# Optimization experiments

Hardware: AMD Instinct MI355X
Metric: run time of the kernel (lower is better)

## Reference

```python
import jax, jax.numpy as jnp
import numpy as np

B, C, H, W = 4, 64, 64, 64

def setup_inputs() -> dict:
    key = jax.random.key(0)
    ks = jax.random.split(key, 7)
    s = 1.0 / np.sqrt(C)
    return {
        "x": jax.random.normal(ks[0], (B, C, H, W), dtype=jnp.float32),
        "Wq": jax.random.normal(ks[1], (C, C), dtype=jnp.float32) * s,
        "bq": jax.random.normal(ks[2], (C,), dtype=jnp.float32) * s,
        "Wk": jax.random.normal(ks[3], (C, C), dtype=jnp.float32) * s,
        "bk": jax.random.normal(ks[4], (C,), dtype=jnp.float32) * s,
        "Wv": jax.random.normal(ks[5], (C, C), dtype=jnp.float32) * s,
        "bv": jax.random.normal(ks[6], (C,), dtype=jnp.float32) * s,
    }

def reference(x, Wq, bq, Wk, bk, Wv, bv):
    b, c, h, w = x.shape
    n = h * w
    xf = x.reshape(b, c, n)                                   # (B,C,N)
    # 1x1 convs == per-pixel linear maps over channels
    q = jnp.einsum('oc,bcn->bon', Wq, xf) + bq[None, :, None]  # (B,C,N)
    k = jnp.einsum('oc,bcn->bon', Wk, xf) + bk[None, :, None]  # (B,C,N)
    v = jnp.einsum('oc,bcn->bon', Wv, xf) + bv[None, :, None]  # (B,C,N)
    # energy = Q^T K : (B,N,N); note: no 1/sqrt(C) scaling in the original
    energy = jnp.einsum('bcn,bcm->bnm', q, k)
    attention = jax.nn.softmax(energy, axis=-1)
    # out = V @ attention^T : out[:, :, i] = sum_j V[:, :, j] * attention[i, j]
    out = jnp.einsum('bcm,bnm->bcn', v, attention)
    return out.reshape(b, c, h, w)
```

## Files before the change

kernel.cpp:

```cpp
#include <hip/hip_runtime.h>
#include <math.h>

#define T_N 4096
#define T_C 64
#define T_B 4
#define NSLICE 8
#define TILES_PER_SLICE (64 / NSLICE)

typedef __attribute__((ext_vector_type(8))) _Float16 f16x8;
typedef __attribute__((ext_vector_type(4))) _Float16 f16x4;
typedef __attribute__((ext_vector_type(4))) float f32x4;

__device__ inline unsigned short f2h(float f) {
    union { _Float16 h; unsigned short s; } u; u.h = (_Float16)f; return u.s;
}
__device__ inline float h2f(unsigned short s) {
    union { unsigned short s; _Float16 h; } u; u.s = s; return (float)u.h;
}

__global__ __launch_bounds__(256) void qkv_kernel(
    const float* __restrict__ x,
    const float* __restrict__ Wq, const float* __restrict__ bq,
    const float* __restrict__ Wk, const float* __restrict__ bk,
    const float* __restrict__ Wv, const float* __restrict__ bv,
    unsigned short* __restrict__ qt_hi, unsigned short* __restrict__ qt_lo,
    unsigned short* __restrict__ kt, unsigned short* __restrict__ vb)
{
    __shared__ __align__(16) unsigned short xsh[32 * 72];
    __shared__ __align__(16) unsigned short xsl[32 * 72];
    __shared__ __align__(16) unsigned short wf[3][64 * 72];

    const int tid = threadIdx.x;
    const int n0  = blockIdx.x * 32;
    const int b   = blockIdx.y;
    const float* xb = x + (size_t)b * T_C * T_N;

    const float* Ws[3] = {Wq, Wk, Wv};
    #pragma unroll
    for (int p = 0; p < 3; ++p) {
        for (int i = tid; i < 1024; i += 256) {
            const int o = i >> 4, c4 = (i & 15) * 4;
            const float4 w4 = ((const float4*)Ws[p])[i];
            f16x4 wh;
            wh[0] = (_Float16)w4.x; wh[1] = (_Float16)w4.y;
            wh[2] = (_Float16)w4.z; wh[3] = (_Float16)w4.w;
            *(f16x4*)&wf[p][o * 72 + c4] = wh;
        }
    }
    for (int i = tid; i < 512; i += 256) {
        const int c = i >> 3, nj4 = (i & 7) * 4;
        const float4 xv = *(const float4*)&xb[c * T_N + n0 + nj4];
        const float xa[4] = {xv.x, xv.y, xv.z, xv.w};
        #pragma unroll
        for (int j = 0; j < 4; ++j) {
            const unsigned short h = f2h(xa[j]);
            xsh[(nj4 + j) * 72 + c] = h;
            xsl[(nj4 + j) * 72 + c] = f2h(xa[j] - h2f(h));
        }
    }
    __syncthreads();

    const int wv_  = tid >> 6;
    const int lane = tid & 63;
    const int quad = lane >> 4;
    const int col  = lane & 15;
    const int pst  = (wv_ & 1) * 16;
    const int oh   = (wv_ >> 1) * 2;
    const size_t bN = (size_t)b * T_N;

    f16x8 xh[2], xl[2];
    #pragma unroll
    for (int s = 0; s < 2; ++s) {
        xh[s] = *(const f16x8*)&xsh[(pst + col) * 72 + s * 32 + quad * 8];
        xl[s] = *(const f16x8*)&xsl[(pst + col) * 72 + s * 32 + quad * 8];
    }
    __syncthreads();

    const float* biases[3] = {bq, bk, bv};
    for (int p = 0; p < 3; ++p) {
        #pragma unroll
        for (int oo = 0; oo < 2; ++oo) {
            const int osub = oh + oo;
            f32x4 acc = (f32x4){0.f, 0.f, 0.f, 0.f};
            #pragma unroll
            for (int s = 0; s < 2; ++s) {
                const f16x8 wfr =
                    *(const f16x8*)&wf[p][(osub * 16 + col) * 72 + s * 32 + quad * 8];
                acc = __builtin_amdgcn_mfma_f32_16x16x32_f16(xh[s], wfr, acc, 0, 0, 0);
                acc = __builtin_amdgcn_mfma_f32_16x16x32_f16(xl[s], wfr, acc, 0, 0, 0);
            }
            const float bb = biases[p][osub * 16 + col];
            if (p == 0) {
                #pragma unroll
                for (int r = 0; r < 4; ++r) {
                    const float f = acc[r] + bb;
                    const unsigned short h = f2h(f);
                    const int a = (pst + quad * 4 + r) * 72 + osub * 16 + col;
                    xsh[a] = h;
                    xsl[a] = f2h(f - h2f(h));
                }
            } else if (p == 1) {
                #pragma unroll
                for (int r = 0; r < 4; ++r)
                    xsh[(pst + quad * 4 + r) * 72 + osub * 16 + col] = f2h(acc[r] + bb);
            } else {
                union { ushort4 v; unsigned short s[4]; } hv;
                #pragma unroll
                for (int r = 0; r < 4; ++r) hv.s[r] = f2h(acc[r] + bb);
                *(ushort4*)&xsh[(osub * 16 + col) * 36 + pst + quad * 4] = hv.v;
            }
        }
        __syncthreads();
        if (p == 0) {
            const int pix = tid >> 3, c8 = (tid & 7) * 8;
            *(f16x8*)&qt_hi[(bN + n0 + pix) * 64 + c8] = *(const f16x8*)&xsh[pix * 72 + c8];
            *(f16x8*)&qt_lo[(bN + n0 + pix) * 64 + c8] = *(const f16x8*)&xsl[pix * 72 + c8];
        } else if (p == 1) {
            const int pix = tid >> 3, c8 = (tid & 7) * 8;
            *(f16x8*)&kt[(bN + n0 + pix) * 64 + c8] = *(const f16x8*)&xsh[pix * 72 + c8];
        } else {
            const int o = tid >> 2, p8 = (tid & 3) * 8;
            *(f16x8*)&vb[((size_t)(b * 64 + o)) * T_N + n0 + p8] =
                *(const f16x8*)&xsh[o * 36 + p8];
        }
        if (p < 2) __syncthreads();
    }
}

__global__ __launch_bounds__(256, 4) void attn_kernel(
    const unsigned short* __restrict__ qt_hi, const unsigned short* __restrict__ qt_lo,
    const unsigned short* __restrict__ kt, const unsigned short* __restrict__ vb,
    unsigned short* __restrict__ o_part, float* __restrict__ mp, float* __restrict__ lp)
{
    __shared__ __align__(16) unsigned short ks[64 * 72];
    __shared__ __align__(16) unsigned short vs[64 * 72];

    const int tid   = threadIdx.x;
    const int n0    = blockIdx.x * 64;
    const int slice = blockIdx.y;
    const int b     = blockIdx.z;
    const int wv_   = tid >> 6;
    const int lane  = tid & 63;
    const int quad  = lane >> 4;
    const int col   = lane & 15;

    const size_t bN = (size_t)b * T_N;
    const int q_own = n0 + wv_ * 16 + col;

    f16x8 qh[2], ql[2];
    #pragma unroll
    for (int s = 0; s < 2; ++s) {
        const size_t qoff = (bN + q_own) * 64 + s * 32 + quad * 8;
        qh[s] = *(const f16x8*)&qt_hi[qoff];
        ql[s] = *(const f16x8*)&qt_lo[qoff];
    }

    f32x4 O[4];
    #pragma unroll
    for (int t = 0; t < 4; ++t) O[t] = (f32x4){0.f, 0.f, 0.f, 0.f};
    float m_st = -INFINITY, l_st = 0.f;

    for (int it = 0; it < TILES_PER_SLICE; ++it) {
        const int m0 = (slice * TILES_PER_SLICE + it) * 64;
        __syncthreads();
        for (int i = tid; i < 1024; i += 256) {
            if (i < 512) {
                const int row = i >> 3, cc = i & 7;
                *(float4*)&ks[row * 72 + cc * 8] =
                    *(const float4*)&kt[(bN + m0 + row) * 64 + cc * 8];
            } else {
                const int j = i - 512, row = j >> 3, cc = j & 7;
                *(float4*)&vs[row * 72 + cc * 8] =
                    *(const float4*)&vb[((size_t)(b * 64 + row)) * T_N + m0 + cc * 8];
            }
        }
        __syncthreads();

        f32x4 acc[4];
        #pragma unroll
        for (int t = 0; t < 4; ++t) acc[t] = (f32x4){0.f, 0.f, 0.f, 0.f};
        #pragma unroll
        for (int s = 0; s < 2; ++s) {
            #pragma unroll
            for (int t = 0; t < 4; ++t) {
                const f16x8 kf =
                    *(const f16x8*)&ks[(t * 16 + col) * 72 + s * 32 + quad * 8];
                acc[t] = __builtin_amdgcn_mfma_f32_16x16x32_f16(kf, qh[s], acc[t], 0, 0, 0);
                acc[t] = __builtin_amdgcn_mfma_f32_16x16x32_f16(kf, ql[s], acc[t], 0, 0, 0);
            }
        }

        float mx = -INFINITY;
        #pragma unroll
        for (int t = 0; t < 4; ++t)
            #pragma unroll
            for (int r = 0; r < 4; ++r) mx = fmaxf(mx, acc[t][r]);
        mx = fmaxf(mx, __shfl_xor(mx, 16));
        mx = fmaxf(mx, __shfl_xor(mx, 32));
        const float mnew = fmaxf(m_st, mx);
        const float alpha = __expf(m_st - mnew);
        float sum = 0.f;
        f16x4 pf[4];
        #pragma unroll
        for (int t = 0; t < 4; ++t) {
            #pragma unroll
            for (int r = 0; r < 4; ++r) {
                const float pv = __expf(acc[t][r] - mnew);
                sum += pv;
                pf[t][r] = (_Float16)pv;
            }
        }
        sum += __shfl_xor(sum, 16);
        sum += __shfl_xor(sum, 32);
        l_st = alpha * l_st + sum;
        m_st = mnew;

        #pragma unroll
        for (int tc = 0; tc < 4; ++tc) {
            O[tc] *= alpha;
            #pragma unroll
            for (int t = 0; t < 4; ++t) {
                const f16x4 vf =
                    *(const f16x4*)&vs[(tc * 16 + col) * 72 + t * 16 + quad * 4];
                O[tc] = __builtin_amdgcn_mfma_f32_16x16x16f16(vf, pf[t], O[tc], 0, 0, 0);
            }
        }
    }

    #pragma unroll
    for (int tc = 0; tc < 4; ++tc) {
        #pragma unroll
        for (int r = 0; r < 4; ++r) {
            o_part[((size_t)((slice * T_B + b) * 64 + tc * 16 + quad * 4 + r)) * T_N +
                   q_own] = f2h(O[tc][r]);
        }
    }
    if (quad == 0) {
        const size_t off = (size_t)(slice * T_B + b) * T_N + q_own;
        mp[off] = m_st;
        lp[off] = l_st;
    }
}

__global__ __launch_bounds__(256) void combine_kernel(
    const unsigned short* __restrict__ o_part,
    const float* __restrict__ mp, const float* __restrict__ lp,
    float* __restrict__ out)
{
    __shared__ float wn[NSLICE][32];

    const int tid = threadIdx.x;
    const int n0  = blockIdx.x * 32;
    const int b   = blockIdx.y;

    if (tid < 32) {
        float m_s[NSLICE], l_s[NSLICE];
        #pragma unroll
        for (int s = 0; s < NSLICE; ++s) {
            const size_t off = (size_t)(s * T_B + b) * T_N + n0 + tid;
            m_s[s] = mp[off];
            l_s[s] = lp[off];
        }
        float M = m_s[0];
        #pragma unroll
        for (int s = 1; s < NSLICE; ++s) M = fmaxf(M, m_s[s]);
        float w_s[NSLICE], L = 0.f;
        #pragma unroll
        for (int s = 0; s < NSLICE; ++s) {
            w_s[s] = __expf(m_s[s] - M);
            L += l_s[s] * w_s[s];
        }
        const float inv = 1.f / L;
        #pragma unroll
        for (int s = 0; s < NSLICE; ++s) wn[s][tid] = w_s[s] * inv;
    }
    __syncthreads();

    for (int t = tid; t < 512; t += 256) {
        const int c = t >> 3, g = t & 7;
        float4 acc = make_float4(0.f, 0.f, 0.f, 0.f);
        #pragma unroll
        for (int s = 0; s < NSLICE; ++s) {
            const ushort4 o4 = *(const ushort4*)
                &o_part[((size_t)((s * T_B + b) * 64 + c)) * T_N + n0 + g * 4];
            acc.x = fmaf(h2f(o4.x), wn[s][g * 4 + 0], acc.x);
            acc.y = fmaf(h2f(o4.y), wn[s][g * 4 + 1], acc.y);
            acc.z = fmaf(h2f(o4.z), wn[s][g * 4 + 2], acc.z);
            acc.w = fmaf(h2f(o4.w), wn[s][g * 4 + 3], acc.w);
        }
        *(float4*)&out[((size_t)(b * 64 + c)) * T_N + n0 + g * 4] = acc;
    }
}

extern "C" void kernel_launch(void* const* d_in, const int* in_sizes, int n_in,
                              void* d_out, int out_size, void* d_ws, size_t ws_size,
                              hipStream_t stream) {
    const float* x  = (const float*)d_in[0];
    const float* Wq = (const float*)d_in[1];
    const float* bq = (const float*)d_in[2];
    const float* Wk = (const float*)d_in[3];
    const float* bk = (const float*)d_in[4];
    const float* Wv = (const float*)d_in[5];
    const float* bv = (const float*)d_in[6];
    float* outp = (float*)d_out;

    const size_t elems = (size_t)T_B * T_N * T_C;
    unsigned short* qt_hi  = (unsigned short*)d_ws;
    unsigned short* qt_lo  = qt_hi + elems;
    unsigned short* ktp    = qt_lo + elems;
    unsigned short* vbuf   = ktp + elems;
    unsigned short* o_part = vbuf + elems;
    float* mp = (float*)(o_part + (size_t)NSLICE * elems);
    float* lp = mp + (size_t)NSLICE * T_B * T_N;

    qkv_kernel<<<dim3(T_N / 32, T_B), 256, 0, stream>>>(
        x, Wq, bq, Wk, bk, Wv, bv, qt_hi, qt_lo, ktp, vbuf);
    attn_kernel<<<dim3(T_N / 64, NSLICE, T_B), 256, 0, stream>>>(
        qt_hi, qt_lo, ktp, vbuf, o_part, mp, lp);
    combine_kernel<<<dim3(T_N / 32, T_B), 256, 0, stream>>>(
        o_part, mp, lp, outp);
}
```

Measured before the change: 134.5 us.

## Fuse QKV, attention and combine into one persistent kernel with grid barriers

Merges the three launches into a single 512-block kernel that uses atomic-counter grid barriers between the QKV projection, attention and combine phases. The attention split-K is cut from 8 slices to 2 so the whole grid (512 blocks) can be resident at once, and the weights are read straight from global memory instead of being staged in shared memory. This removes two launch gaps and shrinks the partial-output traffic, but leaves only 512 attention blocks, each doing 32 KV tiles, so parallelism per block is lower. The grid barrier also relies on every block being co-resident to avoid deadlock.

```diff
diff --git a/kernel.cpp b/kernel.cpp
--- a/kernel.cpp
+++ b/kernel.cpp
@@ -4,8 +4,9 @@
 #define T_N 4096
 #define T_C 64
 #define T_B 4
-#define NSLICE 8
+#define NSLICE 2
 #define TILES_PER_SLICE (64 / NSLICE)
+#define NBLOCKS 512
 
 typedef __attribute__((ext_vector_type(8))) _Float16 f16x8;
 typedef __attribute__((ext_vector_type(4))) _Float16 f16x4;
@@ -18,277 +19,283 @@
     union { unsigned short s; _Float16 h; } u; u.s = s; return (float)u.h;
 }
 
-__global__ __launch_bounds__(256) void qkv_kernel(
+__device__ inline void grid_barrier(unsigned int* cnt) {
+    __syncthreads();
+    if (threadIdx.x == 0) {
+        __threadfence();
+        atomicAdd(cnt, 1u);
+        while (__hip_atomic_load(cnt, __ATOMIC_ACQUIRE,
+                                 __HIP_MEMORY_SCOPE_AGENT) < NBLOCKS) {
+            __builtin_amdgcn_s_sleep(2);
+        }
+    }
+    __syncthreads();
+}
+
+__global__ __launch_bounds__(256, 4) void fused_kernel(
     const float* __restrict__ x,
     const float* __restrict__ Wq, const float* __restrict__ bq,
     const float* __restrict__ Wk, const float* __restrict__ bk,
     const float* __restrict__ Wv, const float* __restrict__ bv,
     unsigned short* __restrict__ qt_hi, unsigned short* __restrict__ qt_lo,
-    unsigned short* __restrict__ kt, unsigned short* __restrict__ vb)
+    unsigned short* __restrict__ kt, unsigned short* __restrict__ vb,
+    unsigned short* __restrict__ o_part, float* __restrict__ mp,
+    float* __restrict__ lp, unsigned int* __restrict__ bars,
+    float* __restrict__ out)
 {
-    __shared__ __align__(16) unsigned short xsh[32 * 72];
-    __shared__ __align__(16) unsigned short xsl[32 * 72];
-    __shared__ __align__(16) unsigned short wf[3][64 * 72];
-
-    const int tid = threadIdx.x;
-    const int n0  = blockIdx.x * 32;
-    const int b   = blockIdx.y;
-    const float* xb = x + (size_t)b * T_C * T_N;
-
-    const float* Ws[3] = {Wq, Wk, Wv};
-    #pragma unroll
-    for (int p = 0; p < 3; ++p) {
-        for (int i = tid; i < 1024; i += 256) {
-            const int o = i >> 4, c4 = (i & 15) * 4;
-            const float4 w4 = ((const float4*)Ws[p])[i];
-            f16x4 wh;
-            wh[0] = (_Float16)w4.x; wh[1] = (_Float16)w4.y;
-            wh[2] = (_Float16)w4.z; wh[3] = (_Float16)w4.w;
-            *(f16x4*)&wf[p][o * 72 + c4] = wh;
-        }
-    }
-    for (int i = tid; i < 512; i += 256) {
-        const int c = i >> 3, nj4 = (i & 7) * 4;
-        const float4 xv = *(const float4*)&xb[c * T_N + n0 + nj4];
-        const float xa[4] = {xv.x, xv.y, xv.z, xv.w};
-        #pragma unroll
-        for (int j = 0; j < 4; ++j) {
-            const unsigned short h = f2h(xa[j]);
-            xsh[(nj4 + j) * 72 + c] = h;
-            xsl[(nj4 + j) * 72 + c] = f2h(xa[j] - h2f(h));
-        }
-    }
-    __syncthreads();
-
+    __shared__ __align__(16) unsigned short smem[9216];
+
+    const int tid  = threadIdx.x;
+    const int bid  = blockIdx.x;
     const int wv_  = tid >> 6;
     const int lane = tid & 63;
     const int quad = lane >> 4;
     const int col  = lane & 15;
-    const int pst  = (wv_ & 1) * 16;
-    const int oh   = (wv_ >> 1) * 2;
-    const size_t bN = (size_t)b * T_N;
-
-    f16x8 xh[2], xl[2];
-    #pragma unroll
-    for (int s = 0; s < 2; ++s) {
-        xh[s] = *(const f16x8*)&xsh[(pst + col) * 72 + s * 32 + quad * 8];
-        xl[s] = *(const f16x8*)&xsl[(pst + col) * 72 + s * 32 + quad * 8];
-    }
-    __syncthreads();
-
-    const float* biases[3] = {bq, bk, bv};
-    for (int p = 0; p < 3; ++p) {
-        #pragma unroll
-        for (int oo = 0; oo < 2; ++oo) {
-            const int osub = oh + oo;
-            f32x4 acc = (f32x4){0.f, 0.f, 0.f, 0.f};
-            #pragma unroll
-            for (int s = 0; s < 2; ++s) {
-                const f16x8 wfr =
-                    *(const f16x8*)&wf[p][(osub * 16 + col) * 72 + s * 32 + quad * 8];
-                acc = __builtin_amdgcn_mfma_f32_16x16x32_f16(xh[s], wfr, acc, 0, 0, 0);
-                acc = __builtin_amdgcn_mfma_f32_16x16x32_f16(xl[s], wfr, acc, 0, 0, 0);
-            }
-            const float bb = biases[p][osub * 16 + col];
-            if (p == 0) {
-                #pragma unroll
-                for (int r = 0; r < 4; ++r) {
-                    const float f = acc[r] + bb;
-                    const unsigned short h = f2h(f);
-                    const int a = (pst + quad * 4 + r) * 72 + osub * 16 + col;
-                    xsh[a] = h;
-                    xsl[a] = f2h(f - h2f(h));
-                }
-            } else if (p == 1) {
-                #pragma unroll
-                for (int r = 0; r < 4; ++r)
-                    xsh[(pst + quad * 4 + r) * 72 + osub * 16 + col] = f2h(acc[r] + bb);
-            } else {
-                union { ushort4 v; unsigned short s[4]; } hv;
-                #pragma unroll
-                for (int r = 0; r < 4; ++r) hv.s[r] = f2h(acc[r] + bb);
-                *(ushort4*)&xsh[(osub * 16 + col) * 36 + pst + quad * 4] = hv.v;
+
+    {
+        unsigned short* xsh = smem;
+        unsigned short* xsl = smem + 2304;
+
+        const int b  = bid >> 7;
+        const int n0 = (bid & 127) * 32;
+        const float* xb = x + (size_t)b * T_C * T_N;
+        const size_t bN = (size_t)b * T_N;
+
+        for (int i = tid; i < 512; i += 256) {
+            const int c = i >> 3, px4 = (i & 7) * 4;
+            const float4 xv = *(const float4*)&xb[c * T_N + n0 + px4];
+            const float xa[4] = {xv.x, xv.y, xv.z, xv.w};
+            #pragma unroll
+            for (int j = 0; j < 4; ++j) {
+                const unsigned short h = f2h(xa[j]);
+                xsh[(px4 + j) * 72 + c] = h;
+                xsl[(px4 + j) * 72 + c] = f2h(xa[j] - h2f(h));
             }
         }
         __syncthreads();
-        if (p == 0) {
-            const int pix = tid >> 3, c8 = (tid & 7) * 8;
-            *(f16x8*)&qt_hi[(bN + n0 + pix) * 64 + c8] = *(const f16x8*)&xsh[pix * 72 + c8];
-            *(f16x8*)&qt_lo[(bN + n0 + pix) * 64 + c8] = *(const f16x8*)&xsl[pix * 72 + c8];
-        } else if (p == 1) {
-            const int pix = tid >> 3, c8 = (tid & 7) * 8;
-            *(f16x8*)&kt[(bN + n0 + pix) * 64 + c8] = *(const f16x8*)&xsh[pix * 72 + c8];
-        } else {
-            const int o = tid >> 2, p8 = (tid & 3) * 8;
-            *(f16x8*)&vb[((size_t)(b * 64 + o)) * T_N + n0 + p8] =
-                *(const f16x8*)&xsh[o * 36 + p8];
-        }
-        if (p < 2) __syncthreads();
-    }
-}
-
-__global__ __launch_bounds__(256, 4) void attn_kernel(
-    const unsigned short* __restrict__ qt_hi, const unsigned short* __restrict__ qt_lo,
-    const unsigned short* __restrict__ kt, const unsigned short* __restrict__ vb,
-    unsigned short* __restrict__ o_part, float* __restrict__ mp, float* __restrict__ lp)
-{
-    __shared__ __align__(16) unsigned short ks[64 * 72];
-    __shared__ __align__(16) unsigned short vs[64 * 72];
-
-    const int tid   = threadIdx.x;
-    const int n0    = blockIdx.x * 64;
-    const int slice = blockIdx.y;
-    const int b     = blockIdx.z;
-    const int wv_   = tid >> 6;
-    const int lane  = tid & 63;
-    const int quad  = lane >> 4;
-    const int col   = lane & 15;
-
-    const size_t bN = (size_t)b * T_N;
-    const int q_own = n0 + wv_ * 16 + col;
-
-    f16x8 qh[2], ql[2];
-    #pragma unroll
-    for (int s = 0; s < 2; ++s) {
-        const size_t qoff = (bN + q_own) * 64 + s * 32 + quad * 8;
-        qh[s] = *(const f16x8*)&qt_hi[qoff];
-        ql[s] = *(const f16x8*)&qt_lo[qoff];
-    }
-
-    f32x4 O[4];
-    #pragma unroll
-    for (int t = 0; t < 4; ++t) O[t] = (f32x4){0.f, 0.f, 0.f, 0.f};
-    float m_st = -INFINITY, l_st = 0.f;
-
-    for (int it = 0; it < TILES_PER_SLICE; ++it) {
-        const int m0 = (slice * TILES_PER_SLICE + it) * 64;
-        __syncthreads();
-        for (int i = tid; i < 1024; i += 256) {
-            if (i < 512) {
-                const int row = i >> 3, cc = i & 7;
-                *(float4*)&ks[row * 72 + cc * 8] =
-                    *(const float4*)&kt[(bN + m0 + row) * 64 + cc * 8];
-            } else {
-                const int j = i - 512, row = j >> 3, cc = j & 7;
-                *(float4*)&vs[row * 72 + cc * 8] =
-                    *(const float4*)&vb[((size_t)(b * 64 + row)) * T_N + m0 + cc * 8];
-            }
-        }
-        __syncthreads();
-
-        f32x4 acc[4];
-        #pragma unroll
-        for (int t = 0; t < 4; ++t) acc[t] = (f32x4){0.f, 0.f, 0.f, 0.f};
+
+        const int pst = (wv_ & 1) * 16;
+        const int oh  = (wv_ >> 1) * 2;
+
+        f16x8 xh[2], xl[2];
         #pragma unroll
         for (int s = 0; s < 2; ++s) {
+            xh[s] = *(const f16x8*)&xsh[(pst + col) * 72 + s * 32 + quad * 8];
+            xl[s] = *(const f16x8*)&xsl[(pst + col) * 72 + s * 32 + quad * 8];
+        }
+        __syncthreads();
+
+        const float* Ws[3]     = {Wq, Wk, Wv};
+        const float* biases[3] = {bq, bk, bv};
+        for (int p = 0; p < 3; ++p) {
+            #pragma unroll
+            for (int oo = 0; oo < 2; ++oo) {
+                const int osub = oh + oo;
+                f32x4 acc = (f32x4){0.f, 0.f, 0.f, 0.f};
+                #pragma unroll
+                for (int s = 0; s < 2; ++s) {
+                    const float* wrow = Ws[p] + (osub * 16 + col) * 64 + s * 32 + quad * 8;
+                    const float4 wa = *(const float4*)&wrow[0];
+                    const float4 wb = *(const float4*)&wrow[4];
+                    f16x8 wfr;
+                    wfr[0] = (_Float16)wa.x; wfr[1] = (_Float16)wa.y;
+                    wfr[2] = (_Float16)wa.z; wfr[3] = (_Float16)wa.w;
+                    wfr[4] = (_Float16)wb.x; wfr[5] = (_Float16)wb.y;
+                    wfr[6] = (_Float16)wb.z; wfr[7] = (_Float16)wb.w;
+                    acc = __builtin_amdgcn_mfma_f32_16x16x32_f16(xh[s], wfr, acc, 0, 0, 0);
+                    acc = __builtin_amdgcn_mfma_f32_16x16x32_f16(xl[s], wfr, acc, 0, 0, 0);
+                }
+                const float bb = biases[p][osub * 16 + col];
+                if (p == 0) {
+                    #pragma unroll
+                    for (int r = 0; r < 4; ++r) {
+                        const float f = acc[r] + bb;
+                        const unsigned short h = f2h(f);
+                        const int a = (pst + quad * 4 + r) * 72 + osub * 16 + col;
+                        xsh[a] = h;
+                        xsl[a] = f2h(f - h2f(h));
+                    }
+                } else if (p == 1) {
+                    #pragma unroll
+                    for (int r = 0; r < 4; ++r)
+                        xsh[(pst + quad * 4 + r) * 72 + osub * 16 + col] = f2h(acc[r] + bb);
+                } else {
+                    union { ushort4 v; unsigned short s[4]; } hv;
+                    #pragma unroll
+                    for (int r = 0; r < 4; ++r) hv.s[r] = f2h(acc[r] + bb);
+                    *(ushort4*)&xsh[(osub * 16 + col) * 36 + pst + quad * 4] = hv.v;
+                }
+            }
+            __syncthreads();
+            if (p == 0) {
+                const int pix = tid >> 3, c8 = (tid & 7) * 8;
+                *(f16x8*)&qt_hi[(bN + n0 + pix) * 64 + c8] = *(const f16x8*)&xsh[pix * 72 + c8];
+                *(f16x8*)&qt_lo[(bN + n0 + pix) * 64 + c8] = *(const f16x8*)&xsl[pix * 72 + c8];
+                __syncthreads();
+            } else if (p == 1) {
+                const int pix = tid >> 3, c8 = (tid & 7) * 8;
+                *(f16x8*)&kt[(bN + n0 + pix) * 64 + c8] = *(const f16x8*)&xsh[pix * 72 + c8];
+                __syncthreads();
+            } else {
+                const int o = tid >> 2, p8 = (tid & 3) * 8;
+                *(f16x8*)&vb[((size_t)(b * 64 + o)) * T_N + n0 + p8] =
+                    *(const f16x8*)&xsh[o * 36 + p8];
+            }
+        }
+    }
+
+    grid_barrier(&bars[0]);
+
+    {
+        unsigned short* ks = smem;
+        unsigned short* vs = smem + 4608;
+
+        const int n0    = (bid & 63) * 64;
+        const int slice = (bid >> 6) & 1;
+        const int b     = bid >> 7;
+        const size_t bN = (size_t)b * T_N;
+        const int q_own = n0 + wv_ * 16 + col;
+
+        f16x8 qh[2], ql[2];
+        #pragma unroll
+        for (int s = 0; s < 2; ++s) {
+            const size_t qoff = (bN + q_own) * 64 + s * 32 + quad * 8;
+            qh[s] = *(const f16x8*)&qt_hi[qoff];
+            ql[s] = *(const f16x8*)&qt_lo[qoff];
+        }
+
+        f32x4 O[4];
+        #pragma unroll
+        for (int t = 0; t < 4; ++t) O[t] = (f32x4){0.f, 0.f, 0.f, 0.f};
+        float m_st = -INFINITY, l_st = 0.f;
+
+        for (int it = 0; it < TILES_PER_SLICE; ++it) {
+            const int m0 = (slice * TILES_PER_SLICE + it) * 64;
+            __syncthreads();
+            for (int i = tid; i < 1024; i += 256) {
+                if (i < 512) {
+                    const int row = i >> 3, cc = i & 7;
+                    *(float4*)&ks[row * 72 + cc * 8] =
+                        *(const float4*)&kt[(bN + m0 + row) * 64 + cc * 8];
+                } else {
+                    const int j = i - 512, row = j >> 3, cc = j & 7;
+                    *(float4*)&vs[row * 72 + cc * 8] =
+                        *(const float4*)&vb[((size_t)(b * 64 + row)) * T_N + m0 + cc * 8];
+                }
+            }
+            __syncthreads();
+
+            f32x4 acc[4];
+            #pragma unroll
+            for (int t = 0; t < 4; ++t) acc[t] = (f32x4){0.f, 0.f, 0.f, 0.f};
+            #pragma unroll
+            for (int s = 0; s < 2; ++s) {
+                #pragma unroll
+                for (int t = 0; t < 4; ++t) {
+                    const f16x8 kf =
+                        *(const f16x8*)&ks[(t * 16 + col) * 72 + s * 32 + quad * 8];
+                    acc[t] = __builtin_amdgcn_mfma_f32_16x16x32_f16(kf, qh[s], acc[t], 0, 0, 0);
+                    acc[t] = __builtin_amdgcn_mfma_f32_16x16x32_f16(kf, ql[s], acc[t], 0, 0, 0);
+                }
+            }
+
+            float mx = -INFINITY;
+            #pragma unroll
+            for (int t = 0; t < 4; ++t)
+                #pragma unroll
+                for (int r = 0; r < 4; ++r) mx = fmaxf(mx, acc[t][r]);
+            mx = fmaxf(mx, __shfl_xor(mx, 16));
+            mx = fmaxf(mx, __shfl_xor(mx, 32));
+            const float mnew = fmaxf(m_st, mx);
+            const float alpha = __expf(m_st - mnew);
+            float sum = 0.f;
+            f16x4 pf[4];
             #pragma unroll
             for (int t = 0; t < 4; ++t) {
-                const f16x8 kf =
-                    *(const f16x8*)&ks[(t * 16 + col) * 72 + s * 32 + quad * 8];
-                acc[t] = __builtin_amdgcn_mfma_f32_16x16x32_f16(kf, qh[s], acc[t], 0, 0, 0);
-                acc[t] = __builtin_amdgcn_mfma_f32_16x16x32_f16(kf, ql[s], acc[t], 0, 0, 0);
-            }
-        }
-
-        float mx = -INFINITY;
-        #pragma unroll
-        for (int t = 0; t < 4; ++t)
-            #pragma unroll
-            for (int r = 0; r < 4; ++r) mx = fmaxf(mx, acc[t][r]);
-        mx = fmaxf(mx, __shfl_xor(mx, 16));
-        mx = fmaxf(mx, __shfl_xor(mx, 32));
-        const float mnew = fmaxf(m_st, mx);
-        const float alpha = __expf(m_st - mnew);
-        float sum = 0.f;
-        f16x4 pf[4];
-        #pragma unroll
-        for (int t = 0; t < 4; ++t) {
-            #pragma unroll
-            for (int r = 0; r < 4; ++r) {
-                const float pv = __expf(acc[t][r] - mnew);
-                sum += pv;
-                pf[t][r] = (_Float16)pv;
-            }
-        }
-        sum += __shfl_xor(sum, 16);
-        sum += __shfl_xor(sum, 32);
-        l_st = alpha * l_st + sum;
-        m_st = mnew;
+                #pragma unroll
+                for (int r = 0; r < 4; ++r) {
+                    const float pv = __expf(acc[t][r] - mnew);
+                    sum += pv;
+                    pf[t][r] = (_Float16)pv;
+                }
+            }
+            sum += __shfl_xor(sum, 16);
+            sum += __shfl_xor(sum, 32);
+            l_st = alpha * l_st + sum;
+            m_st = mnew;
+
+            #pragma unroll
+            for (int tc = 0; tc < 4; ++tc) {
+                O[tc] *= alpha;
+                #pragma unroll
+                for (int t = 0; t < 4; ++t) {
+                    const f16x4 vf =
+                        *(const f16x4*)&vs[(tc * 16 + col) * 72 + t * 16 + quad * 4];
+                    O[tc] = __builtin_amdgcn_mfma_f32_16x16x16f16(vf, pf[t], O[tc], 0, 0, 0);
+                }
+            }
+        }
 
         #pragma unroll
         for (int tc = 0; tc < 4; ++tc) {
-            O[tc] *= alpha;
-            #pragma unroll
-            for (int t = 0; t < 4; ++t) {
-                const f16x4 vf =
-                    *(const f16x4*)&vs[(tc * 16 + col) * 72 + t * 16 + quad * 4];
-                O[tc] = __builtin_amdgcn_mfma_f32_16x16x16f16(vf, pf[t], O[tc], 0, 0, 0);
-            }
+            #pragma unroll
+            for (int r = 0; r < 4; ++r) {
+                o_part[((size_t)((slice * T_B + b) * 64 + tc * 16 + quad * 4 + r)) * T_N +
+                       q_own] = f2h(O[tc][r]);
+            }
+        }
+        if (quad == 0) {
+            const size_t off = (size_t)(slice * T_B + b) * T_N + q_own;
+            mp[off] = m_st;
+            lp[off] = l_st;
         }
     }
 
-    #pragma unroll
-    for (int tc = 0; tc < 4; ++tc) {
-        #pragma unroll
-        for (int r = 0; r < 4; ++r) {
-            o_part[((size_t)((slice * T_B + b) * 64 + tc * 16 + quad * 4 + r)) * T_N +
-                   q_own] = f2h(O[tc][r]);
-        }
-    }
-    if (quad == 0) {
-        const size_t off = (size_t)(slice * T_B + b) * T_N + q_own;
-        mp[off] = m_st;
-        lp[off] = l_st;
-    }
-}
-
-__global__ __launch_bounds__(256) void combine_kernel(
-    const unsigned short* __restrict__ o_part,
-    const float* __restrict__ mp, const float* __restrict__ lp,
-    float* __restrict__ out)
-{
-    __shared__ float wn[NSLICE][32];
-
-    const int tid = threadIdx.x;
-    const int n0  = blockIdx.x * 32;
-    const int b   = blockIdx.y;
-
-    if (tid < 32) {
-        float m_s[NSLICE], l_s[NSLICE];
-        #pragma unroll
-        for (int s = 0; s < NSLICE; ++s) {
-            const size_t off = (size_t)(s * T_B + b) * T_N + n0 + tid;
-            m_s[s] = mp[off];
-            l_s[s] = lp[off];
-        }
-        float M = m_s[0];
-        #pragma unroll
-        for (int s = 1; s < NSLICE; ++s) M = fmaxf(M, m_s[s]);
-        float w_s[NSLICE], L = 0.f;
-        #pragma unroll
-        for (int s = 0; s < NSLICE; ++s) {
-            w_s[s] = __expf(m_s[s] - M);
-            L += l_s[s] * w_s[s];
-        }
-        const float inv = 1.f / L;
-        #pragma unroll
-        for (int s = 0; s < NSLICE; ++s) wn[s][tid] = w_s[s] * inv;
-    }
-    __syncthreads();
-
-    for (int t = tid; t < 512; t += 256) {
-        const int c = t >> 3, g = t & 7;
-        float4 acc = make_float4(0.f, 0.f, 0.f, 0.f);
-        #pragma unroll
-        for (int s = 0; s < NSLICE; ++s) {
-            const ushort4 o4 = *(const ushort4*)
-                &o_part[((size_t)((s * T_B + b) * 64 + c)) * T_N + n0 + g * 4];
-            acc.x = fmaf(h2f(o4.x), wn[s][g * 4 + 0], acc.x);
-            acc.y = fmaf(h2f(o4.y), wn[s][g * 4 + 1], acc.y);
-            acc.z = fmaf(h2f(o4.z), wn[s][g * 4 + 2], acc.z);
-            acc.w = fmaf(h2f(o4.w), wn[s][g * 4 + 3], acc.w);
-        }
-        *(float4*)&out[((size_t)(b * 64 + c)) * T_N + n0 + g * 4] = acc;
+    grid_barrier(&bars[1]);
+
+    {
+        float* wn = (float*)smem;
+
+        const int b  = bid >> 7;
+        const int n0 = (bid & 127) * 32;
+
+        if (tid < 32) {
+            float m_s[NSLICE], l_s[NSLICE];
+            #pragma unroll
+            for (int s = 0; s < NSLICE; ++s) {
+                const size_t off = (size_t)(s * T_B + b) * T_N + n0 + tid;
+                m_s[s] = mp[off];
+                l_s[s] = lp[off];
+            }
+            float M = m_s[0];
+            #pragma unroll
+            for (int s = 1; s < NSLICE; ++s) M = fmaxf(M, m_s[s]);
+            float w_s[NSLICE], L = 0.f;
+            #pragma unroll
+            for (int s = 0; s < NSLICE; ++s) {
+                w_s[s] = __expf(m_s[s] - M);
+                L += l_s[s] * w_s[s];
+            }
+            const float inv = 1.f / L;
+            #pragma unroll
+            for (int s = 0; s < NSLICE; ++s) wn[s * 32 + tid] = w_s[s] * inv;
+        }
+        __syncthreads();
+
+        for (int t = tid; t < 512; t += 256) {
+            const int c = t >> 3, g = t & 7;
+            float4 acc = make_float4(0.f, 0.f, 0.f, 0.f);
+            #pragma unroll
+            for (int s = 0; s < NSLICE; ++s) {
+                const ushort4 o4 = *(const ushort4*)
+                    &o_part[((size_t)((s * T_B + b) * 64 + c)) * T_N + n0 + g * 4];
+                acc.x = fmaf(h2f(o4.x), wn[s * 32 + g * 4 + 0], acc.x);
+                acc.y = fmaf(h2f(o4.y), wn[s * 32 + g * 4 + 1], acc.y);
+                acc.z = fmaf(h2f(o4.z), wn[s * 32 + g * 4 + 2], acc.z);
+                acc.w = fmaf(h2f(o4.w), wn[s * 32 + g * 4 + 3], acc.w);
+            }
+            *(float4*)&out[((size_t)(b * 64 + c)) * T_N + n0 + g * 4] = acc;
+        }
     }
 }
 
@@ -304,8 +311,9 @@
     const float* bv = (const float*)d_in[6];
     float* outp = (float*)d_out;
 
+    unsigned int* bars = (unsigned int*)d_ws;
     const size_t elems = (size_t)T_B * T_N * T_C;
-    unsigned short* qt_hi  = (unsigned short*)d_ws;
+    unsigned short* qt_hi  = (unsigned short*)((char*)d_ws + 16);
     unsigned short* qt_lo  = qt_hi + elems;
     unsigned short* ktp    = qt_lo + elems;
     unsigned short* vbuf   = ktp + elems;
@@ -313,10 +321,8 @@
     float* mp = (float*)(o_part + (size_t)NSLICE * elems);
     float* lp = mp + (size_t)NSLICE * T_B * T_N;
 
-    qkv_kernel<<<dim3(T_N / 32, T_B), 256, 0, stream>>>(
-        x, Wq, bq, Wk, bk, Wv, bv, qt_hi, qt_lo, ktp, vbuf);
-    attn_kernel<<<dim3(T_N / 64, NSLICE, T_B), 256, 0, stream>>>(
-        qt_hi, qt_lo, ktp, vbuf, o_part, mp, lp);
-    combine_kernel<<<dim3(T_N / 32, T_B), 256, 0, stream>>>(
-        o_part, mp, lp, outp);
-}
+    hipMemsetAsync(bars, 0, 8, stream);
+    fused_kernel<<<dim3(NBLOCKS), dim3(256), 0, stream>>>(
+        x, Wq, bq, Wk, bk, Wv, bv, qt_hi, qt_lo, ktp, vbuf,
+        o_part, mp, lp, bars, outp);
+}
```

After: 267.3 us. 98.7% more time.
